# Optimization experiments

Measured on AMD Instinct MI355X. Metric: run time of the kernel, lower is better.

The kernel has to match this reference:

```python
import jax, jax.numpy as jnp
import numpy as np

B, N, C_IN = 4, 4096, 64
DIM = 64
NKP = 15
K = 32               # neighbor_limits
CONV_RADIUS = 0.1 * 2.0   # conv_radius * rigid_scale (is_deform=False)
KERNEL_RADIUS = 0.12
RECEP = 1.2          # kernel_point_receptive_radius
TRANS_DIM = 128
INF = 1000000.0


def _square_distance(src, dst):
    # src [B,N,3], dst [B,M,3] -> [B,N,M]
    d = -2.0 * jnp.einsum('bnc,bmc->bnm', src, dst)
    d = d + jnp.sum(src * src, -1)[:, :, None]
    d = d + jnp.sum(dst * dst, -1)[:, None, :]
    return d


def _query_ball(xyz, radius):
    # xyz [B,N,3] -> neighbor idx [B,N,K]; out-of-radius mapped to N (shadow)
    n = xyz.shape[1]
    sq = _square_distance(xyz, xyz)
    idx = jnp.broadcast_to(jnp.arange(n, dtype=jnp.int32), sq.shape)
    idx = jnp.where(sq > radius * radius, n, idx)
    idx = jnp.sort(idx, axis=-1)[:, :, :K]
    return idx


def _index_points(points_bcn, idx, pad_val):
    # points [B,C,N], idx [B,N,K] -> [B,N,K,C]; index N hits shadow row = pad_val
    p = jnp.transpose(points_bcn, (0, 2, 1))          # [B,N,C]
    shadow = jnp.full((p.shape[0], 1, p.shape[2]), pad_val, p.dtype)
    p = jnp.concatenate([p, shadow], axis=1)          # [B,N+1,C]
    b_idx = jnp.arange(p.shape[0])[:, None, None]
    return p[b_idx, idx]                              # [B,N,K,C]


def setup_inputs() -> dict:
    key = jax.random.key(0)
    ks = jax.random.split(key, 12)
    pos = jax.random.uniform(ks[0], (B, 3, N), dtype=jnp.float32)
    feat = jax.random.normal(ks[1], (B, C_IN, N), dtype=jnp.float32)
    # kernel points: center point at origin, rest inside kernel_radius ball ('center' mode)
    kp_rest = jax.random.uniform(ks[2], (3, NKP - 1), minval=-KERNEL_RADIUS,
                                 maxval=KERNEL_RADIUS, dtype=jnp.float32)
    kp_pos = jnp.concatenate([jnp.zeros((3, 1), jnp.float32), kp_rest], axis=1)  # [3,NKP]
    s = 0.05
    cb_w = jax.random.normal(ks[3], (DIM, C_IN), jnp.float32) * s
    cb_b = jax.random.normal(ks[4], (DIM,), jnp.float32) * s
    kp_weight = jax.random.normal(ks[5], (NKP, DIM, DIM), jnp.float32) * s
    kp_bias = jax.random.normal(ks[6], (DIM,), jnp.float32) * s
    ce_w = jax.random.normal(ks[7], (C_IN, DIM), jnp.float32) * s
    ce_b = jax.random.normal(ks[8], (C_IN,), jnp.float32) * s
    f1_w = jax.random.normal(ks[9], (2 * DIM, 2 * DIM), jnp.float32) * s
    f1_b = jnp.zeros((2 * DIM,), jnp.float32)
    f2_w = jax.random.normal(ks[10], (TRANS_DIM, 2 * DIM), jnp.float32) * s
    f2_b = jnp.zeros((TRANS_DIM,), jnp.float32)
    return dict(pos=pos, feat=feat, kp_pos=kp_pos, cb_w=cb_w, cb_b=cb_b,
                kp_weight=kp_weight, kp_bias=kp_bias, ce_w=ce_w, ce_b=ce_b,
                f1_w=f1_w, f1_b=f1_b, f2_w=f2_w, f2_b=f2_b)


def reference(pos, feat, kp_pos, cb_w, cb_b, kp_weight, kp_bias, ce_w, ce_b,
              f1_w, f1_b, f2_w, f2_b):
    xyz = jnp.transpose(jax.lax.stop_gradient(pos), (0, 2, 1))       # [B,N,3]
    neighbor_idx = _query_ball(xyz, CONV_RADIUS)                     # [B,N,K]
    # NOTE: with is_deform=False the original code does NOT subtract the center
    # position; rel_neighbor_pos is the absolute gathered positions.
    neighbor_pos = jnp.transpose(_index_points(pos, neighbor_idx, INF),
                                 (0, 3, 1, 2))                        # [B,3,N,K]
    feat0 = jnp.einsum('oc,bcn->bon', cb_w, feat) + cb_b[None, :, None]
    neighbor_feat = _index_points(feat0, neighbor_idx, 0.0)           # [B,N,K,DIM]

    kp_pos_deform = kp_pos.reshape(1, 3, 1, NKP) + 0.0                # offset = 0
    diff = neighbor_pos[..., None] - kp_pos_deform[:, :, :, None, :]  # [B,3,N,K,NKP]
    sq_d = jnp.sum(diff * diff, axis=1)                               # [B,N,K,NKP]
    w = jnp.clip(1.0 - jnp.sqrt(sq_d) / RECEP, 0.0)                   # [B,N,K,NKP]
    w = jnp.transpose(w, (0, 1, 3, 2))                                # [B,N,NKP,K]
    weighted = jnp.einsum('bnpk,bnkc->bnpc', w, neighbor_feat)        # [B,N,NKP,DIM]
    out = jnp.einsum('bnpc,pcd->bnd', weighted, kp_weight) + kp_bias  # [B,N,DIM]
    out = jax.nn.relu(jnp.transpose(out, (0, 2, 1)))                  # [B,DIM,N]
    out = jax.nn.relu(jnp.einsum('oc,bcn->bon', ce_w, out)
                      + ce_b[None, :, None] + feat)                   # [B,C_IN,N]

    fuse_in = jnp.concatenate(
        [jnp.transpose(weighted, (0, 3, 1, 2)),                       # [B,DIM,N,NKP]
         jnp.broadcast_to(out[..., None], (B, DIM, N, NKP))], axis=1) # [B,2DIM,N,NKP]
    h = jax.nn.relu(jnp.einsum('oc,bcnk->bonk', f1_w, fuse_in)
                    + f1_b[None, :, None, None])
    fuse = jax.nn.relu(jnp.einsum('oc,bcnk->bonk', f2_w, h)
                       + f2_b[None, :, None, None])                   # [B,TRANS_DIM,N,NKP]
    return out, kp_pos_deform, fuse
```

## Files before the change

### kernel.cpp

```cpp
#include <hip/hip_runtime.h>
#include <hip/hip_bf16.h>
#include <stdint.h>

#define NPTS 4096
#define NB   4
#define KNN  32
#define NKPT 15

#define OFF_IDX      0ULL
#define OFF_FEAT0    2097152ULL
#define OFF_WEIGHTED 6292480ULL
#define OFF_HO       37749760ULL
#define OFF_W1P      46138368ULL
#define OFF_W2P      46171136ULL
#define OFF_KPWP     46203904ULL

#define OUT_OFF_OUT  0
#define OUT_OFF_KP   1048576
#define OUT_OFF_FUSE 1048621

#define SBU(u) ((u) ^ (((u) >> 3) & 7))

typedef __attribute__((ext_vector_type(8))) short short8v;
typedef __attribute__((ext_vector_type(4))) float f32x4;

__device__ __forceinline__ unsigned short bf16b(float f) {
  __hip_bfloat16 h = __float2bfloat16(f);
  return *(unsigned short*)&h;
}
__device__ __forceinline__ unsigned pkbf(float lo, float hi) {
  return (unsigned)bf16b(lo) | ((unsigned)bf16b(hi) << 16);
}

__global__ __launch_bounds__(256) void k012(const float* __restrict__ pos,
                                            const float* __restrict__ feat,
                                            const float* __restrict__ cb_w,
                                            const float* __restrict__ cb_b,
                                            const float* __restrict__ f1_w,
                                            const float* __restrict__ f2_w,
                                            const float* __restrict__ kpw,
                                            const float* __restrict__ kp_pos,
                                            int* __restrict__ idx_ws,
                                            float* __restrict__ feat0,
                                            unsigned short* __restrict__ w1p,
                                            unsigned short* __restrict__ w2p,
                                            unsigned short* __restrict__ kpwp,
                                            float* __restrict__ out_kp) {
  __shared__ float cbt[64 * 65];
  const int blk = blockIdx.x;
  if (blk < 4096) {
    const int w = threadIdx.x >> 6, lane = threadIdx.x & 63;
    const int pt = blk * 4 + w;
    const int b = pt >> 12, n = pt & 4095;
    const float* px = pos + (size_t)b * 3 * NPTS;
    const double x0 = (double)px[n], y0 = (double)px[NPTS + n], z0 = (double)px[2 * NPTS + n];
    const double ssrc = x0 * x0 + y0 * y0 + z0 * z0;
    const double RAD = 0.1 * 2.0;
    const double R2 = RAD * RAD;
    int cnt = 0;
    int* op = idx_ws + (size_t)pt * KNN;
    for (int ch = 0; ch < 64; ++ch) {
      const int j = ch * 64 + lane;
      const double xj = (double)px[j], yj = (double)px[NPTS + j], zj = (double)px[2 * NPTS + j];
      const double dot  = x0 * xj + y0 * yj + z0 * zj;
      const double sdst = xj * xj + yj * yj + zj * zj;
      const double sq = -2.0 * dot + ssrc + sdst;
      const bool keep = !(sq > R2);
      const unsigned long long m = __ballot(keep);
      if (keep) {
        const int p = cnt + (int)__popcll(m & ((1ULL << lane) - 1ULL));
        if (p < KNN) op[p] = j;
      }
      cnt += (int)__popcll(m);
      if (cnt >= KNN) break;
    }
    const int s = cnt + lane;
    if (s < KNN) op[s] = NPTS;
    return;
  }
  if (blk < 8192) {
    const int t = threadIdx.x;
    #pragma unroll
    for (int q = 0; q < 16; ++q) {
      const int idx = q * 256 + t;
      const int d = idx >> 6, c = idx & 63;
      cbt[c * 65 + d] = cb_w[idx];
    }
    __syncthreads();
    const int ptl = t >> 6, d = t & 63;
    const int pt = (blk - 4096) * 4 + ptl;
    const int b = pt >> 12, n = pt & 4095;
    const float* fp = feat + (size_t)b * 64 * NPTS + n;
    float acc = 0.f;
    #pragma unroll
    for (int c = 0; c < 64; ++c) acc = fmaf(cbt[c * 65 + d], fp[(size_t)c * NPTS], acc);
    acc += cb_b[d];
    feat0[((size_t)b * (NPTS + 1) + n) * 64 + d] = acc;
    return;
  }
  int t = (blk - 8192) * 256 + threadIdx.x;
  if (t < 32768) {
    const int w = t >> 14;
    const int i = t & 16383;
    const int j = i & 7, l = (i >> 3) & 63, kc = (i >> 9) & 3, ot = i >> 11;
    const int o = ot * 16 + (l & 15);
    const int k = kc * 32 + (l >> 4) * 8 + j;
    const float* src = w ? f2_w : f1_w;
    unsigned short* dst = w ? w2p : w1p;
    dst[i] = bf16b(src[o * 128 + k]);
    return;
  }
  t -= 32768;
  if (t < 61440) {
    const int j = t & 7, l = (t >> 3) & 63, nt = (t >> 9) & 3, kc = t >> 11;
    const int k = kc * 32 + (l >> 4) * 8 + j;
    const int d = nt * 16 + (l & 15);
    kpwp[t] = bf16b(kpw[(size_t)k * 64 + d]);
    return;
  }
  t -= 61440;
  if (t < NB * 64) { int b = t >> 6, d = t & 63; feat0[((size_t)b * (NPTS + 1) + NPTS) * 64 + d] = 0.f; return; }
  t -= NB * 64;
  if (t < 45) out_kp[t] = kp_pos[t];
}

__global__ __launch_bounds__(256) void k3_weighted(const float* __restrict__ pos,
                                                   const int* __restrict__ idx_ws,
                                                   const float* __restrict__ feat0,
                                                   const float* __restrict__ kp_pos,
                                                   unsigned short* __restrict__ wbf) {
  __shared__ int   nidx[4][KNN];
  __shared__ float npx[4][KNN], npy[4][KNN], npz[4][KNN];
  __shared__ float kp[48];
  __shared__ float wl[4][KNN * 16];
  const int wv = threadIdx.x >> 6, lane = threadIdx.x & 63;
  const int pt = blockIdx.x * 4 + wv;
  const int b = pt >> 12;
  if (threadIdx.x < 45) kp[threadIdx.x] = kp_pos[threadIdx.x];
  if (lane < KNN) {
    const int ki = idx_ws[(size_t)pt * KNN + lane];
    nidx[wv][lane] = ki;
    const bool v = ki < NPTS;
    const float* px = pos + (size_t)b * 3 * NPTS;
    npx[wv][lane] = v ? px[ki] : 1000000.0f;
    npy[wv][lane] = v ? px[NPTS + ki] : 1000000.0f;
    npz[wv][lane] = v ? px[2 * NPTS + ki] : 1000000.0f;
  }
  __syncthreads();
  #pragma unroll
  for (int r = 0; r < 8; ++r) {
    const int i = r * 64 + lane;
    const int k = i >> 4, p = i & 15;
    float wvv = 0.f;
    if (p < 15) {
      const float dx = npx[wv][k] - kp[p];
      const float dy = npy[wv][k] - kp[15 + p];
      const float dz = npz[wv][k] - kp[30 + p];
      const float d2 = dx * dx + dy * dy + dz * dz;
      wvv = fmaxf(1.0f - sqrtf(d2) / 1.2f, 0.f);
    }
    wl[wv][i] = wvv;
  }
  __syncthreads();
  float acc[16];
  #pragma unroll
  for (int p = 0; p < 16; ++p) acc[p] = 0.f;
  const float* f0 = feat0 + (size_t)b * (NPTS + 1) * 64 + lane;
  for (int k = 0; k < KNN; ++k) {
    const float f = f0[(size_t)nidx[wv][k] * 64];
    #pragma unroll
    for (int q = 0; q < 4; ++q) {
      const float4 w4 = *(const float4*)&wl[wv][k * 16 + q * 4];
      acc[q * 4 + 0] = fmaf(w4.x, f, acc[q * 4 + 0]);
      acc[q * 4 + 1] = fmaf(w4.y, f, acc[q * 4 + 1]);
      acc[q * 4 + 2] = fmaf(w4.z, f, acc[q * 4 + 2]);
      acc[q * 4 + 3] = fmaf(w4.w, f, acc[q * 4 + 3]);
    }
  }
  unsigned short* wp = wbf + (size_t)pt * NKPT * 64 + lane;
  #pragma unroll
  for (int p = 0; p < 15; ++p) wp[(size_t)p * 64] = bf16b(acc[p]);
}

__global__ __launch_bounds__(256) void k45(const unsigned short* __restrict__ wbf,
                                           const unsigned short* __restrict__ kpwp,
                                           const float* __restrict__ kp_bias,
                                           const float* __restrict__ ce_w,
                                           const float* __restrict__ ce_b,
                                           const float* __restrict__ feat,
                                           const unsigned short* __restrict__ w1p,
                                           const float* __restrict__ f1_b,
                                           float* __restrict__ out,
                                           float* __restrict__ hO) {
  __shared__ float r0[64 * 65];
  __shared__ float cwt[64 * 64];
  __shared__ unsigned short outT[64 * 74];
  const int t = threadIdx.x;
  const int b = blockIdx.x >> 6;
  const int n0 = (blockIdx.x & 63) * 64;
  const int wv = t >> 6, lane = t & 63;
  #pragma unroll
  for (int q = 0; q < 16; ++q) {
    const int idx = q * 256 + t;
    cwt[idx] = ce_w[(idx & 63) * 64 + (idx >> 6)];
  }
  const short8v* kf = (const short8v*)kpwp;
  f32x4 acc[4];
  #pragma unroll
  for (int nt = 0; nt < 4; ++nt) acc[nt] = (f32x4){0.f, 0.f, 0.f, 0.f};
  const int m0 = b * 4096 + n0 + wv * 16;
  const unsigned short* ap = wbf + (size_t)(m0 + (lane & 15)) * 960 + (lane >> 4) * 8;
  #pragma unroll 6
  for (int kc = 0; kc < 30; ++kc) {
    const short8v a = *(const short8v*)&ap[kc * 32];
    #pragma unroll
    for (int nt = 0; nt < 4; ++nt)
      acc[nt] = __builtin_amdgcn_mfma_f32_16x16x32_bf16(a, kf[(kc * 4 + nt) * 64 + lane], acc[nt], 0, 0, 0);
  }
  const int rl = wv * 16 + (lane >> 4) * 4;
  #pragma unroll
  for (int nt = 0; nt < 4; ++nt) {
    const int d = nt * 16 + (lane & 15);
    const float bv = kp_bias[d];
    #pragma unroll
    for (int r = 0; r < 4; ++r)
      r0[(rl + r) * 65 + d] = fmaxf(acc[nt][r] + bv, 0.f);
  }
  __syncthreads();
  const int nl = t & 63, og = t >> 6;
  float facc[16];
  #pragma unroll
  for (int j = 0; j < 16; ++j) facc[j] = 0.f;
  for (int c = 0; c < 64; ++c) {
    const float x = r0[nl * 65 + c];
    #pragma unroll
    for (int q = 0; q < 4; ++q) {
      const float4 w4 = *(const float4*)&cwt[c * 64 + og * 16 + q * 4];
      facc[q * 4 + 0] = fmaf(w4.x, x, facc[q * 4 + 0]);
      facc[q * 4 + 1] = fmaf(w4.y, x, facc[q * 4 + 1]);
      facc[q * 4 + 2] = fmaf(w4.z, x, facc[q * 4 + 2]);
      facc[q * 4 + 3] = fmaf(w4.w, x, facc[q * 4 + 3]);
    }
  }
  #pragma unroll
  for (int q = 0; q < 4; ++q) {
    const float4 cb4 = *(const float4*)&ce_b[og * 16 + q * 4];
    const float cbv[4] = {cb4.x, cb4.y, cb4.z, cb4.w};
    #pragma unroll
    for (int j = 0; j < 4; ++j) {
      const int o = og * 16 + q * 4 + j;
      const float fv = feat[((size_t)b * 64 + o) * 4096 + n0 + nl];
      const float v = fmaxf((facc[q * 4 + j] + cbv[j]) + fv, 0.f);
      out[((size_t)b * 64 + o) * 4096 + n0 + nl] = v;
      outT[o * 74 + nl] = bf16b(v);
    }
  }
  __syncthreads();
  const short8v* w1f = (const short8v*)w1p;
  f32x4 hacc[8];
  #pragma unroll
  for (int ot = 0; ot < 8; ++ot) hacc[ot] = (f32x4){0.f, 0.f, 0.f, 0.f};
  const int nw = lane & 15;
  #pragma unroll
  for (int kc2 = 0; kc2 < 2; ++kc2) {
    short8v bfr;
    #pragma unroll
    for (int j = 0; j < 8; ++j)
      bfr[j] = (short)outT[(kc2 * 32 + (lane >> 4) * 8 + j) * 74 + wv * 16 + nw];
    #pragma unroll
    for (int ot = 0; ot < 8; ++ot)
      hacc[ot] = __builtin_amdgcn_mfma_f32_16x16x32_bf16(w1f[(ot * 4 + 2 + kc2) * 64 + lane], bfr, hacc[ot], 0, 0, 0);
  }
  const int rb = (lane >> 4) * 4;
  float* hp = hO + ((size_t)b * 4096 + n0 + wv * 16 + nw) * 128;
  #pragma unroll
  for (int ot = 0; ot < 8; ++ot) {
    const float4 b1 = *(const float4*)&f1_b[ot * 16 + rb];
    const float bv[4] = {b1.x, b1.y, b1.z, b1.w};
    #pragma unroll
    for (int r = 0; r < 4; ++r)
      hp[ot * 16 + rb + r] = hacc[ot][r] + bv[r];
  }
}

__global__ __launch_bounds__(256, 2) void k6_fuse(const unsigned short* __restrict__ wbf,
                                                  const float* __restrict__ hO,
                                                  const unsigned short* __restrict__ w1p,
                                                  const unsigned short* __restrict__ w2p,
                                                  const float* __restrict__ f2_b,
                                                  float* __restrict__ fuse) {
  __shared__ __attribute__((aligned(16))) unsigned short SB[16384];
  __shared__ __attribute__((aligned(16))) float hOS[12 * 128];
  const int t = threadIdx.x;
  const int blk = blockIdx.x;
  const int b = blk / 480;
  const int ml0 = (blk - b * 480) * 128;
  const size_t M0 = (size_t)blk * 128;
  const int wv = t >> 6, lane = t & 63;
  const short8v* w1f = (const short8v*)w1p;
  const short8v* w2f = (const short8v*)w2p;

  short8v w1r[16];
  #pragma unroll
  for (int ot = 0; ot < 8; ++ot)
    #pragma unroll
    for (int kc = 0; kc < 2; ++kc)
      w1r[ot * 2 + kc] = w1f[(ot * 4 + kc) * 64 + lane];

  #pragma unroll
  for (int q = 0; q < 4; ++q) {
    const int chunk = q * 256 + t;
    const int m = chunk >> 3, a = chunk & 7;
    const uint4 pk = *(const uint4*)&wbf[(M0 + m) * 64 + a * 8];
    const int kc = a >> 2, hi = a & 3;
    const int u = ((m >> 4) * 4 + kc) * 64 + hi * 16 + (m & 15);
    *(uint4*)&SB[SBU(u) * 8] = pk;
  }
  const int nmin = ml0 / 15;
  #pragma unroll
  for (int q = 0; q < 6; ++q) {
    const int idx = q * 256 + t;
    const int row = idx >> 7, o = idx & 127;
    int n = nmin + row;
    if (n > 4095) n = 4095;
    hOS[idx] = hO[((size_t)b * 4096 + n) * 128 + o];
  }
  __syncthreads();

  short8v xf[4];
  #pragma unroll
  for (int mt = 0; mt < 2; ++mt)
    #pragma unroll
    for (int kc = 0; kc < 2; ++kc) {
      const int u = ((wv * 2 + mt) * 4 + kc) * 64 + lane;
      xf[mt * 2 + kc] = *(const short8v*)&SB[SBU(u) * 8];
    }

  const int rb = (lane >> 4) * 4;
  const int dnA = (ml0 + wv * 32 + (lane & 15)) / 15 - nmin;
  const int dnB = (ml0 + wv * 32 + 16 + (lane & 15)) / 15 - nmin;
  f32x4 acc[8][2];
  #pragma unroll
  for (int ot = 0; ot < 8; ++ot) {
    acc[ot][0] = *(const f32x4*)&hOS[dnA * 128 + ot * 16 + rb];
    acc[ot][1] = *(const f32x4*)&hOS[dnB * 128 + ot * 16 + rb];
  }
  #pragma unroll
  for (int kc = 0; kc < 2; ++kc) {
    #pragma unroll
    for (int ot = 0; ot < 8; ++ot) {
      acc[ot][0] = __builtin_amdgcn_mfma_f32_16x16x32_bf16(w1r[ot * 2 + kc], xf[kc],     acc[ot][0], 0, 0, 0);
      acc[ot][1] = __builtin_amdgcn_mfma_f32_16x16x32_bf16(w1r[ot * 2 + kc], xf[2 + kc], acc[ot][1], 0, 0, 0);
    }
  }
  short8v w2r[32];
  #pragma unroll
  for (int i = 0; i < 32; ++i) w2r[i] = w2f[i * 64 + lane];

  #pragma unroll
  for (int ot = 0; ot < 8; ++ot) {
    const int o0 = ot * 16 + rb;
    const int kc = o0 >> 5, hi = (o0 >> 3) & 3, j0 = o0 & 7;
    #pragma unroll
    for (int mt = 0; mt < 2; ++mt) {
      const f32x4 h = acc[ot][mt];
      const float h0 = fmaxf(h[0], 0.f);
      const float h1 = fmaxf(h[1], 0.f);
      const float h2 = fmaxf(h[2], 0.f);
      const float h3 = fmaxf(h[3], 0.f);
      const int u = ((wv * 2 + mt) * 4 + kc) * 64 + hi * 16 + (lane & 15);
      uint2 pk;
      pk.x = pkbf(h0, h1);
      pk.y = pkbf(h2, h3);
      *(uint2*)&SB[SBU(u) * 8 + j0] = pk;
    }
  }
  short8v hf[8];
  #pragma unroll
  for (int mt = 0; mt < 2; ++mt)
    #pragma unroll
    for (int kc = 0; kc < 4; ++kc) {
      const int u = ((wv * 2 + mt) * 4 + kc) * 64 + lane;
      hf[mt * 4 + kc] = *(const short8v*)&SB[SBU(u) * 8];
    }
  __syncthreads();
  #pragma unroll
  for (int ot = 0; ot < 8; ++ot) {
    acc[ot][0] = (f32x4){0.f, 0.f, 0.f, 0.f};
    acc[ot][1] = (f32x4){0.f, 0.f, 0.f, 0.f};
  }
  #pragma unroll
  for (int kc = 0; kc < 4; ++kc) {
    #pragma unroll
    for (int ot = 0; ot < 8; ++ot) {
      acc[ot][0] = __builtin_amdgcn_mfma_f32_16x16x32_bf16(w2r[ot * 4 + kc], hf[kc],     acc[ot][0], 0, 0, 0);
      acc[ot][1] = __builtin_amdgcn_mfma_f32_16x16x32_bf16(w2r[ot * 4 + kc], hf[4 + kc], acc[ot][1], 0, 0, 0);
    }
  }
  float* SBf = (float*)SB;
  const int colw = wv * 32 + (lane & 15);
  float* fblk = fuse + (size_t)b * 128 * 61440 + ml0;
  #pragma unroll
  for (int p = 0; p < 4; ++p) {
    #pragma unroll
    for (int oi = 0; oi < 2; ++oi) {
      const int ot = p * 2 + oi;
      const int o0 = ot * 16 + rb;
      const float4 b2 = *(const float4*)&f2_b[o0];
      const float bv[4] = {b2.x, b2.y, b2.z, b2.w};
      #pragma unroll
      for (int mt = 0; mt < 2; ++mt) {
        const f32x4 v = acc[ot][mt];
        #pragma unroll
        for (int r = 0; r < 4; ++r)
          SBf[(oi * 16 + rb + r) * 132 + colw + mt * 16] = fmaxf(v[r] + bv[r], 0.f);
      }
    }
    __syncthreads();
    #pragma unroll
    for (int q = 0; q < 16; ++q) {
      const int idx = q * 256 + t;
      const int row = idx >> 7, c = idx & 127;
      fblk[(size_t)(p * 32 + row) * 61440 + c] = SBf[row * 132 + c];
    }
    __syncthreads();
  }
}

extern "C" void kernel_launch(void* const* d_in, const int* in_sizes, int n_in,
                              void* d_out, int out_size, void* d_ws, size_t ws_size,
                              hipStream_t stream) {
  const float* pos     = (const float*)d_in[0];
  const float* feat    = (const float*)d_in[1];
  const float* kp_pos  = (const float*)d_in[2];
  const float* cb_w    = (const float*)d_in[3];
  const float* cb_b    = (const float*)d_in[4];
  const float* kpw     = (const float*)d_in[5];
  const float* kp_bias = (const float*)d_in[6];
  const float* ce_w    = (const float*)d_in[7];
  const float* ce_b    = (const float*)d_in[8];
  const float* f1_w    = (const float*)d_in[9];
  const float* f1_b    = (const float*)d_in[10];
  const float* f2_w    = (const float*)d_in[11];
  const float* f2_b    = (const float*)d_in[12];
  float* out = (float*)d_out;
  char* ws = (char*)d_ws;
  int*   idx_ws   = (int*)(ws + OFF_IDX);
  float* feat0    = (float*)(ws + OFF_FEAT0);
  unsigned short* wbf  = (unsigned short*)(ws + OFF_WEIGHTED);
  float* hO       = (float*)(ws + OFF_HO);
  unsigned short* w1p  = (unsigned short*)(ws + OFF_W1P);
  unsigned short* w2p  = (unsigned short*)(ws + OFF_W2P);
  unsigned short* kpwp = (unsigned short*)(ws + OFF_KPWP);

  k012<<<8562, 256, 0, stream>>>(pos, feat, cb_w, cb_b, f1_w, f2_w, kpw, kp_pos,
                                 idx_ws, feat0, w1p, w2p, kpwp, out + OUT_OFF_KP);
  k3_weighted<<<4096, 256, 0, stream>>>(pos, idx_ws, feat0, kp_pos, wbf);
  k45<<<256, 256, 0, stream>>>(wbf, kpwp, kp_bias, ce_w, ce_b, feat, w1p, f1_b,
                               out + OUT_OFF_OUT, hO);
  k6_fuse<<<1920, 256, 0, stream>>>(wbf, hO, w1p, w2p, f2_b, out + OUT_OFF_FUSE);
}
```

Measured before the change: 137.3 us.

## Store hidden projection in bf16 and write fuse output directly from registers

The per-point hidden projection hO shrinks from fp32 to bf16, which halves the workspace traffic between k45 and k6_fuse and the shared-memory staging in k6_fuse. k6_fuse now loads the w2 weights in two halves to lower register pressure and drops one barrier. The fuse output is written straight from the MFMA accumulators to global memory instead of being transposed through LDS, so the stores are less coalesced (16-wide contiguous runs) but the LDS passes and syncs go away. The bf16 rounding of hO adds some precision loss.

Result: no change. 137.1 us (-0.1%).

```diff
diff --git a/kernel.cpp b/kernel.cpp
--- a/kernel.cpp
+++ b/kernel.cpp
@@ -11,9 +11,9 @@
 #define OFF_FEAT0    2097152ULL
 #define OFF_WEIGHTED 6292480ULL
 #define OFF_HO       37749760ULL
-#define OFF_W1P      46138368ULL
-#define OFF_W2P      46171136ULL
-#define OFF_KPWP     46203904ULL
+#define OFF_W1P      41944064ULL
+#define OFF_W2P      41976832ULL
+#define OFF_KPWP     42009600ULL
 
 #define OUT_OFF_OUT  0
 #define OUT_OFF_KP   1048576
@@ -31,6 +31,8 @@
 __device__ __forceinline__ unsigned pkbf(float lo, float hi) {
   return (unsigned)bf16b(lo) | ((unsigned)bf16b(hi) << 16);
 }
+__device__ __forceinline__ float bflo(unsigned u) { return __uint_as_float(u << 16); }
+__device__ __forceinline__ float bfhi(unsigned u) { return __uint_as_float(u & 0xffff0000u); }
 
 __global__ __launch_bounds__(256) void k012(const float* __restrict__ pos,
                                             const float* __restrict__ feat,
@@ -191,7 +193,7 @@
                                            const unsigned short* __restrict__ w1p,
                                            const float* __restrict__ f1_b,
                                            float* __restrict__ out,
-                                           float* __restrict__ hO) {
+                                           unsigned short* __restrict__ hOb) {
   __shared__ float r0[64 * 65];
   __shared__ float cwt[64 * 64];
   __shared__ unsigned short outT[64 * 74];
@@ -272,25 +274,26 @@
       hacc[ot] = __builtin_amdgcn_mfma_f32_16x16x32_bf16(w1f[(ot * 4 + 2 + kc2) * 64 + lane], bfr, hacc[ot], 0, 0, 0);
   }
   const int rb = (lane >> 4) * 4;
-  float* hp = hO + ((size_t)b * 4096 + n0 + wv * 16 + nw) * 128;
+  unsigned short* hp = hOb + ((size_t)b * 4096 + n0 + wv * 16 + nw) * 128;
   #pragma unroll
   for (int ot = 0; ot < 8; ++ot) {
-    const float4 b1 = *(const float4*)&f1_b[ot * 16 + rb];
-    const float bv[4] = {b1.x, b1.y, b1.z, b1.w};
-    #pragma unroll
-    for (int r = 0; r < 4; ++r)
-      hp[ot * 16 + rb + r] = hacc[ot][r] + bv[r];
+    const int o0 = ot * 16 + rb;
+    const float4 b1 = *(const float4*)&f1_b[o0];
+    uint2 pk;
+    pk.x = pkbf(hacc[ot][0] + b1.x, hacc[ot][1] + b1.y);
+    pk.y = pkbf(hacc[ot][2] + b1.z, hacc[ot][3] + b1.w);
+    *(uint2*)&hp[o0] = pk;
   }
 }
 
 __global__ __launch_bounds__(256, 2) void k6_fuse(const unsigned short* __restrict__ wbf,
-                                                  const float* __restrict__ hO,
+                                                  const unsigned short* __restrict__ hOb,
                                                   const unsigned short* __restrict__ w1p,
                                                   const unsigned short* __restrict__ w2p,
                                                   const float* __restrict__ f2_b,
                                                   float* __restrict__ fuse) {
   __shared__ __attribute__((aligned(16))) unsigned short SB[16384];
-  __shared__ __attribute__((aligned(16))) float hOS[12 * 128];
+  __shared__ __attribute__((aligned(8))) unsigned short hOS[12 * 128];
   const int t = threadIdx.x;
   const int blk = blockIdx.x;
   const int b = blk / 480;
@@ -318,12 +321,12 @@
   }
   const int nmin = ml0 / 15;
   #pragma unroll
-  for (int q = 0; q < 6; ++q) {
+  for (int q = 0; q < 3; ++q) {
     const int idx = q * 256 + t;
-    const int row = idx >> 7, o = idx & 127;
+    const int row = idx >> 6, pr = idx & 63;
     int n = nmin + row;
     if (n > 4095) n = 4095;
-    hOS[idx] = hO[((size_t)b * 4096 + n) * 128 + o];
+    ((unsigned*)hOS)[idx] = ((const unsigned*)(hOb + ((size_t)b * 4096 + n) * 128))[pr];
   }
   __syncthreads();
 
@@ -342,9 +345,15 @@
   f32x4 acc[8][2];
   #pragma unroll
   for (int ot = 0; ot < 8; ++ot) {
-    acc[ot][0] = *(const f32x4*)&hOS[dnA * 128 + ot * 16 + rb];
-    acc[ot][1] = *(const f32x4*)&hOS[dnB * 128 + ot * 16 + rb];
-  }
+    const uint2 pa = *(const uint2*)&hOS[dnA * 128 + ot * 16 + rb];
+    const uint2 pb = *(const uint2*)&hOS[dnB * 128 + ot * 16 + rb];
+    acc[ot][0] = (f32x4){bflo(pa.x), bfhi(pa.x), bflo(pa.y), bfhi(pa.y)};
+    acc[ot][1] = (f32x4){bflo(pb.x), bfhi(pb.x), bflo(pb.y), bfhi(pb.y)};
+  }
+  short8v w2a[16];
+  #pragma unroll
+  for (int i = 0; i < 16; ++i) w2a[i] = w2f[i * 64 + lane];
+
   #pragma unroll
   for (int kc = 0; kc < 2; ++kc) {
     #pragma unroll
@@ -353,10 +362,6 @@
       acc[ot][1] = __builtin_amdgcn_mfma_f32_16x16x32_bf16(w1r[ot * 2 + kc], xf[2 + kc], acc[ot][1], 0, 0, 0);
     }
   }
-  short8v w2r[32];
-  #pragma unroll
-  for (int i = 0; i < 32; ++i) w2r[i] = w2f[i * 64 + lane];
-
   #pragma unroll
   for (int ot = 0; ot < 8; ++ot) {
     const int o0 = ot * 16 + rb;
@@ -375,6 +380,10 @@
       *(uint2*)&SB[SBU(u) * 8 + j0] = pk;
     }
   }
+  short8v w2b[16];
+  #pragma unroll
+  for (int i = 0; i < 16; ++i) w2b[i] = w2f[(16 + i) * 64 + lane];
+
   short8v hf[8];
   #pragma unroll
   for (int mt = 0; mt < 2; ++mt)
@@ -383,7 +392,6 @@
       const int u = ((wv * 2 + mt) * 4 + kc) * 64 + lane;
       hf[mt * 4 + kc] = *(const short8v*)&SB[SBU(u) * 8];
     }
-  __syncthreads();
   #pragma unroll
   for (int ot = 0; ot < 8; ++ot) {
     acc[ot][0] = (f32x4){0.f, 0.f, 0.f, 0.f};
@@ -392,38 +400,32 @@
   #pragma unroll
   for (int kc = 0; kc < 4; ++kc) {
     #pragma unroll
-    for (int ot = 0; ot < 8; ++ot) {
-      acc[ot][0] = __builtin_amdgcn_mfma_f32_16x16x32_bf16(w2r[ot * 4 + kc], hf[kc],     acc[ot][0], 0, 0, 0);
-      acc[ot][1] = __builtin_amdgcn_mfma_f32_16x16x32_bf16(w2r[ot * 4 + kc], hf[4 + kc], acc[ot][1], 0, 0, 0);
-    }
-  }
-  float* SBf = (float*)SB;
-  const int colw = wv * 32 + (lane & 15);
-  float* fblk = fuse + (size_t)b * 128 * 61440 + ml0;
-  #pragma unroll
-  for (int p = 0; p < 4; ++p) {
-    #pragma unroll
-    for (int oi = 0; oi < 2; ++oi) {
-      const int ot = p * 2 + oi;
-      const int o0 = ot * 16 + rb;
-      const float4 b2 = *(const float4*)&f2_b[o0];
-      const float bv[4] = {b2.x, b2.y, b2.z, b2.w};
+    for (int ot = 0; ot < 4; ++ot) {
+      acc[ot][0] = __builtin_amdgcn_mfma_f32_16x16x32_bf16(w2a[ot * 4 + kc], hf[kc],     acc[ot][0], 0, 0, 0);
+      acc[ot][1] = __builtin_amdgcn_mfma_f32_16x16x32_bf16(w2a[ot * 4 + kc], hf[4 + kc], acc[ot][1], 0, 0, 0);
+    }
+  }
+  #pragma unroll
+  for (int kc = 0; kc < 4; ++kc) {
+    #pragma unroll
+    for (int ot = 4; ot < 8; ++ot) {
+      acc[ot][0] = __builtin_amdgcn_mfma_f32_16x16x32_bf16(w2b[(ot - 4) * 4 + kc], hf[kc],     acc[ot][0], 0, 0, 0);
+      acc[ot][1] = __builtin_amdgcn_mfma_f32_16x16x32_bf16(w2b[(ot - 4) * 4 + kc], hf[4 + kc], acc[ot][1], 0, 0, 0);
+    }
+  }
+  float* fp0 = fuse + (size_t)b * 128 * 61440 + ml0 + wv * 32 + (lane & 15);
+  #pragma unroll
+  for (int ot = 0; ot < 8; ++ot) {
+    const int o0 = ot * 16 + rb;
+    const float4 b2 = *(const float4*)&f2_b[o0];
+    const float bv[4] = {b2.x, b2.y, b2.z, b2.w};
+    #pragma unroll
+    for (int mt = 0; mt < 2; ++mt) {
+      const f32x4 vacc = acc[ot][mt];
       #pragma unroll
-      for (int mt = 0; mt < 2; ++mt) {
-        const f32x4 v = acc[ot][mt];
-        #pragma unroll
-        for (int r = 0; r < 4; ++r)
-          SBf[(oi * 16 + rb + r) * 132 + colw + mt * 16] = fmaxf(v[r] + bv[r], 0.f);
-      }
-    }
-    __syncthreads();
-    #pragma unroll
-    for (int q = 0; q < 16; ++q) {
-      const int idx = q * 256 + t;
-      const int row = idx >> 7, c = idx & 127;
-      fblk[(size_t)(p * 32 + row) * 61440 + c] = SBf[row * 132 + c];
-    }
-    __syncthreads();
+      for (int r = 0; r < 4; ++r)
+        fp0[(size_t)(o0 + r) * 61440 + mt * 16] = fmaxf(vacc[r] + bv[r], 0.f);
+    }
   }
 }
 
@@ -448,7 +450,7 @@
   int*   idx_ws   = (int*)(ws + OFF_IDX);
   float* feat0    = (float*)(ws + OFF_FEAT0);
   unsigned short* wbf  = (unsigned short*)(ws + OFF_WEIGHTED);
-  float* hO       = (float*)(ws + OFF_HO);
+  unsigned short* hOb  = (unsigned short*)(ws + OFF_HO);
   unsigned short* w1p  = (unsigned short*)(ws + OFF_W1P);
   unsigned short* w2p  = (unsigned short*)(ws + OFF_W2P);
   unsigned short* kpwp = (unsigned short*)(ws + OFF_KPWP);
@@ -457,6 +459,6 @@
                                  idx_ws, feat0, w1p, w2p, kpwp, out + OUT_OFF_KP);
   k3_weighted<<<4096, 256, 0, stream>>>(pos, idx_ws, feat0, kp_pos, wbf);
   k45<<<256, 256, 0, stream>>>(wbf, kpwp, kp_bias, ce_w, ce_b, feat, w1p, f1_b,
-                               out + OUT_OFF_OUT, hO);
-  k6_fuse<<<1920, 256, 0, stream>>>(wbf, hO, w1p, w2p, f2_b, out + OUT_OFF_FUSE);
-}
+                               out + OUT_OFF_OUT, hOb);
+  k6_fuse<<<1920, 256, 0, stream>>>(wbf, hOb, w1p, w2p, f2_b, out + OUT_OFF_FUSE);
+}
```
